# Performance work log

Measured on AMD Instinct MI355X. Metric: run time of the kernel, lower is better.

## Reference

```python
import jax, jax.numpy as jnp
import numpy as np

NUM_HEADS = 16


def setup_inputs() -> dict:
    key = jax.random.key(0)
    ks = jax.random.split(key, 5)
    N, L, E = 4, 1024, 1024
    x = jax.random.normal(ks[0], (N, L, E), dtype=jnp.float32)
    sc = 1.0 / np.sqrt(E)
    wq = jax.random.normal(ks[1], (E, E), dtype=jnp.float32) * sc
    wk = jax.random.normal(ks[2], (E, E), dtype=jnp.float32) * sc
    wv = jax.random.normal(ks[3], (E, E), dtype=jnp.float32) * sc
    wo = jax.random.normal(ks[4], (E, E), dtype=jnp.float32) * sc
    return {"x": x, "wq": wq, "wk": wk, "wv": wv, "wo": wo}


def reference(x, wq, wk, wv, wo):
    N, L, E = x.shape
    H = NUM_HEADS
    d = E // H  # d_k = d_v = d_q
    # Linear layers: y = x @ W^T (torch Linear weight is (out, in))
    q = (x @ wq.T).reshape(N, H, L, d)  # NOTE: raw view, matches torch .view
    k = (x @ wk.T).reshape(N, H, L, d)
    v = (x @ wv.T).reshape(N, H, L, d)
    scores = jnp.einsum("nhld,nhmd->nhlm", q, k) / jnp.sqrt(jnp.float32(d))
    # causal mask (dropout is identity in eval / p=0)
    causal = jnp.tril(jnp.ones((L, L), dtype=bool))
    scores = jnp.where(causal, scores, jnp.float32(-jnp.inf))
    attn = jax.nn.softmax(scores, axis=-1)
    wei = jnp.einsum("nhlm,nhmd->nhld", attn, v).reshape(N, L, H * d)
    return wei @ wo.T
```

## Files before the change

kernel.cpp:

```cpp
#include <hip/hip_runtime.h>
#include <hip/hip_bf16.h>

using bf16 = __hip_bfloat16;
typedef __attribute__((ext_vector_type(8))) short bf16x8;
typedef __attribute__((ext_vector_type(4))) float f32x4;

#define MFMA16(a, b, c) __builtin_amdgcn_mfma_f32_16x16x32_bf16(a, b, c, 0, 0, 0)
#define SWZ(row, byteoff) ((byteoff) ^ (((row) & 7) << 4))

__device__ __forceinline__ unsigned short f2b(float f) {
  union { float f; unsigned int u; } c; c.f = f;
  unsigned int r = c.u + 0x7fffu + ((c.u >> 16) & 1u);
  return (unsigned short)(r >> 16);
}
__device__ __forceinline__ float b2f(short b) {
  union { unsigned int u; float f; } c;
  c.u = ((unsigned int)(unsigned short)b) << 16;
  return c.f;
}
__device__ __forceinline__ bf16x8 scale8(bf16x8 v, float s) {
  bf16x8 r;
#pragma unroll
  for (int j = 0; j < 8; ++j) r[j] = (short)f2b(b2f(v[j]) * s);
  return r;
}
__device__ __forceinline__ unsigned cvtpk(float a, float b) {
  unsigned r;
  asm("v_cvt_pk_bf16_f32 %0, %1, %2" : "=v"(r) : "v"(a), "v"(b));
  return r;
}

__device__ __forceinline__ void gload_lds16(const void* g, void* l) {
  __builtin_amdgcn_global_load_lds(
      (const __attribute__((address_space(1))) void*)g,
      (__attribute__((address_space(3))) void*)l, 16, 0, 0);
}

__device__ __forceinline__ void store_out(float* p, float v) { *p = v; }
__device__ __forceinline__ void store_out(bf16* p, float v) {
  *(unsigned short*)p = f2b(v);
}

__global__ __launch_bounds__(256) void cast_all(
    const float* __restrict__ x, const float* __restrict__ wq,
    const float* __restrict__ wk, const float* __restrict__ wv,
    const float* __restrict__ wo,
    unsigned short* __restrict__ xb, unsigned short* __restrict__ wqb,
    unsigned short* __restrict__ wkb, unsigned short* __restrict__ wvb,
    unsigned short* __restrict__ wob) {
  for (int i = blockIdx.x * 256 + threadIdx.x; i < 2097152; i += 2048 * 256) {
    const float* src;
    unsigned short* dst;
    int off;
    if (i < 1048576) {
      src = x; dst = xb; off = i;
    } else {
      int j = i - 1048576;
      int seg = j >> 18;
      off = j & 262143;
      src = (seg == 0) ? wq : (seg == 1) ? wk : (seg == 2) ? wv : wo;
      dst = (seg == 0) ? wqb : (seg == 1) ? wkb : (seg == 2) ? wvb : wob;
    }
    float4 v = reinterpret_cast<const float4*>(src)[off];
    ushort4 o;
    o.x = f2b(v.x); o.y = f2b(v.y); o.z = f2b(v.z); o.w = f2b(v.w);
    reinterpret_cast<ushort4*>(dst)[off] = o;
  }
}

template <typename TOUT>
__device__ __forceinline__ void gemm_tile(const bf16* __restrict__ A,
                                          const bf16* __restrict__ Bt,
                                          TOUT* __restrict__ C, int N, int K,
                                          int bm, int bn) {
  __shared__ bf16 Asm[128 * 64];
  __shared__ bf16 Bsm[128 * 64];
  const int tid = threadIdx.x;
  const int lane = tid & 63;
  const int w = tid >> 6;
  const int wr = w >> 1, wc = w & 1;
  const int fr = lane & 15;
  const int fg = lane >> 4;
  f32x4 acc[4][4] = {};

  const int strow = w * 8 + (lane >> 3);
  const int stcb = (lane & 7) * 16;

  for (int kt = 0; kt < K; kt += 64) {
#pragma unroll
    for (int r = 0; r < 4; ++r) {
      const int row = r * 32 + strow;
      gload_lds16(
          (const char*)(A + (size_t)(bm + row) * K + kt) + SWZ(row, stcb),
          (char*)Asm + (r * 32 + w * 8) * 128);
      gload_lds16(
          (const char*)(Bt + (size_t)row * K + kt) + SWZ(row, stcb),
          (char*)Bsm + (r * 32 + w * 8) * 128);
    }
    __syncthreads();
    bf16x8 afr[4][2], bfr[4][2];
#pragma unroll
    for (int m = 0; m < 4; ++m) {
      const int row = wr * 64 + m * 16 + fr;
      const char* rp = (const char*)Asm + row * 128;
#pragma unroll
      for (int s = 0; s < 2; ++s)
        afr[m][s] = *(const bf16x8*)(rp + SWZ(row, s * 64 + fg * 16));
    }
#pragma unroll
    for (int n = 0; n < 4; ++n) {
      const int row = wc * 64 + n * 16 + fr;
      const char* rp = (const char*)Bsm + row * 128;
#pragma unroll
      for (int s = 0; s < 2; ++s)
        bfr[n][s] = *(const bf16x8*)(rp + SWZ(row, s * 64 + fg * 16));
    }
    __builtin_amdgcn_s_setprio(1);
#pragma unroll
    for (int m = 0; m < 4; ++m)
#pragma unroll
      for (int n = 0; n < 4; ++n) {
        acc[m][n] = MFMA16(afr[m][0], bfr[n][0], acc[m][n]);
        acc[m][n] = MFMA16(afr[m][1], bfr[n][1], acc[m][n]);
      }
    __builtin_amdgcn_s_setprio(0);
    __syncthreads();
  }
#pragma unroll
  for (int m = 0; m < 4; ++m) {
    const int row0 = bm + wr * 64 + m * 16 + (lane >> 4) * 4;
#pragma unroll
    for (int n = 0; n < 4; ++n) {
      const int col = bn + wc * 64 + n * 16 + fr;
#pragma unroll
      for (int r = 0; r < 4; ++r)
        store_out(&C[(size_t)(row0 + r) * N + col], acc[m][n][r]);
    }
  }
}

__global__ __launch_bounds__(256) void gemm_qkv(
    const bf16* __restrict__ A, const bf16* __restrict__ B3,
    bf16* __restrict__ Cq, bf16* __restrict__ Ck, bf16* __restrict__ Cv) {
  const int id = blockIdx.y * 32 + blockIdx.x;
  const int sw = (id & 7) * 96 + (id >> 3);
  const int bm = (sw & 31) * 128;
  const int bnG = (sw >> 5) * 128;
  bf16* C = (bnG < 1024) ? Cq : (bnG < 2048) ? Ck : Cv;
  gemm_tile<bf16>(A, B3 + (size_t)bnG * 1024, C, 1024, 1024, bm, bnG & 1023);
}

__global__ __launch_bounds__(256) void gemm_out64(const bf16* __restrict__ A,
                                                  const bf16* __restrict__ B,
                                                  float* __restrict__ C) {
  __shared__ bf16 Asm[128 * 64];
  __shared__ bf16 Bsm[64 * 64];
  const int id = blockIdx.y * 32 + blockIdx.x;
  const int sw = (id & 7) * 64 + (id >> 3);
  const int bm = (sw & 31) * 128;
  const int bn = (sw >> 5) * 64;
  const bf16* Bt = B + (size_t)bn * 1024;

  const int tid = threadIdx.x;
  const int lane = tid & 63;
  const int w = tid >> 6;
  const int wr = w >> 1, wc = w & 1;
  const int fr = lane & 15;
  const int fg = lane >> 4;
  f32x4 acc[4][2] = {};

  const int strow = w * 8 + (lane >> 3);
  const int stcb = (lane & 7) * 16;

  for (int kt = 0; kt < 1024; kt += 64) {
#pragma unroll
    for (int r = 0; r < 4; ++r) {
      const int row = r * 32 + strow;
      gload_lds16(
          (const char*)(A + (size_t)(bm + row) * 1024 + kt) + SWZ(row, stcb),
          (char*)Asm + (r * 32 + w * 8) * 128);
    }
#pragma unroll
    for (int r = 0; r < 2; ++r) {
      const int row = r * 32 + strow;
      gload_lds16(
          (const char*)(Bt + (size_t)row * 1024 + kt) + SWZ(row, stcb),
          (char*)Bsm + (r * 32 + w * 8) * 128);
    }
    __syncthreads();
    bf16x8 afr[4][2], bfr[2][2];
#pragma unroll
    for (int m = 0; m < 4; ++m) {
      const int row = wr * 64 + m * 16 + fr;
      const char* rp = (const char*)Asm + row * 128;
#pragma unroll
      for (int s = 0; s < 2; ++s)
        afr[m][s] = *(const bf16x8*)(rp + SWZ(row, s * 64 + fg * 16));
    }
#pragma unroll
    for (int n = 0; n < 2; ++n) {
      const int row = wc * 32 + n * 16 + fr;
      const char* rp = (const char*)Bsm + row * 128;
#pragma unroll
      for (int s = 0; s < 2; ++s)
        bfr[n][s] = *(const bf16x8*)(rp + SWZ(row, s * 64 + fg * 16));
    }
    __builtin_amdgcn_s_setprio(1);
#pragma unroll
    for (int m = 0; m < 4; ++m)
#pragma unroll
      for (int n = 0; n < 2; ++n) {
        acc[m][n] = MFMA16(afr[m][0], bfr[n][0], acc[m][n]);
        acc[m][n] = MFMA16(afr[m][1], bfr[n][1], acc[m][n]);
      }
    __builtin_amdgcn_s_setprio(0);
    __syncthreads();
  }
#pragma unroll
  for (int m = 0; m < 4; ++m) {
    const int row0 = bm + wr * 64 + m * 16 + fg * 4;
#pragma unroll
    for (int n = 0; n < 2; ++n) {
      const int col = bn + wc * 32 + n * 16 + fr;
#pragma unroll
      for (int r = 0; r < 4; ++r)
        C[(size_t)(row0 + r) * 1024 + col] = acc[m][n][r];
    }
  }
}

__global__ __launch_bounds__(256) void attn_fwd(
    const bf16* __restrict__ Q, const bf16* __restrict__ K,
    const bf16* __restrict__ V, bf16* __restrict__ O) {
  const int nh = blockIdx.x;
  const size_t base = (size_t)nh * 65536;
  const bf16* Qp = Q + base;
  const bf16* Kp = K + base;
  const bf16* Vp = V + base;
  bf16* Op = O + base;
  const int pmap[8] = {0, 1, 2, 3, 6, 7, 4, 5};
  const int p = pmap[blockIdx.y];
  const int qiA = p, qiB = 15 - p;
  const int tid = threadIdx.x;
  const int lane = tid & 63;
  const int w = tid >> 6;
  const int fr = lane & 15;
  const int fg = lane >> 4;

  __shared__ __align__(16) bf16 Ksm[2][2][64 * 64];
  __shared__ __align__(16) bf16 Vts[2][2][64 * 64];

  const float QSC = 0.125f * 1.44269504089f;
  const float MS = 12.0f;
  const int rA0 = qiA * 64 + w * 16;
  const int rB0 = qiB * 64 + w * 16;
  bf16x8 qA[2], qB[2];
#pragma unroll
  for (int ks = 0; ks < 2; ++ks) {
    qA[ks] = scale8(
        *(const bf16x8*)&Qp[(size_t)(rA0 + fr) * 64 + ks * 32 + fg * 8], QSC);
    qB[ks] = scale8(
        *(const bf16x8*)&Qp[(size_t)(rB0 + fr) * 64 + ks * 32 + fg * 8], QSC);
  }

  float sA = 0.f, sB = 0.f;
  f32x4 oA[4], oB[4];
#pragma unroll
  for (int d = 0; d < 4; ++d) {
    oA[d] = (f32x4){0.f, 0.f, 0.f, 0.f};
    oB[d] = (f32x4){0.f, 0.f, 0.f, 0.f};
  }

  const int NKV = qiB + 1;
  const int qloc = w * 16 + fr;

  const int bkv = (tid & 15) * 4;
  const int bd = (tid >> 4) * 4;
  const int sbk = ((bkv >> 5) << 6) + (((bkv >> 2) & 3) << 4) +
                  (((bkv >> 4) & 1) << 3);
  union VU { ushort4 v; unsigned short s[4]; };
  VU v4a[4], v4b[4];

  const int krow = w * 16 + (lane >> 3);
  const int kcb = (lane & 7) * 16;

#define STAGE_K(kt, dst)                                                      \
  {                                                                           \
    _Pragma("unroll") for (int i = 0; i < 2; ++i) {                           \
      const int row = krow + i * 8;                                           \
      gload_lds16((const char*)Kp + ((size_t)((kt)*64 + row) * 128 +          \
                                     SWZ(row, kcb)),                          \
                  (char*)(dst) + (w * 16 + i * 8) * 128);                     \
    }                                                                         \
  }
#define LOAD_V(kt, r)                                                         \
  {                                                                           \
    _Pragma("unroll") for (int j = 0; j < 4; ++j) (r)[j].v =                  \
        *(const ushort4*)(Vp + (size_t)((kt)*64 + bkv + j) * 64 + bd);        \
  }
#define WRITE_V(dst, r)                                                       \
  {                                                                           \
    _Pragma("unroll") for (int i = 0; i < 4; ++i) {                           \
      VU o4;                                                                  \
      _Pragma("unroll") for (int j = 0; j < 4; ++j) o4.s[j] = (r)[j].s[i];    \
      const int row = bd + i;                                                 \
      *(ushort4*)((char*)(dst) + row * 128 + SWZ(row, sbk)) = o4.v;           \
    }                                                                         \
  }

  union PU { bf16x8 v; unsigned u[4]; };

  auto load_kf = [&](const char* kb, bf16x8 (&kf)[4][2]) {
#pragma unroll
    for (int c = 0; c < 4; ++c) {
      const int row = c * 16 + fr;
      const char* rp = kb + row * 128;
      kf[c][0] = *(const bf16x8*)(rp + SWZ(row, fg * 16));
      kf[c][1] = *(const bf16x8*)(rp + SWZ(row, 64 + fg * 16));
    }
  };
  auto load_vf = [&](const char* vb, bf16x8 (&vf)[4][2]) {
#pragma unroll
    for (int d = 0; d < 4; ++d) {
      const int row = d * 16 + fr;
      const char* rp = vb + row * 128;
#pragma unroll
      for (int ks = 0; ks < 2; ++ks)
        vf[d][ks] = *(const bf16x8*)(rp + SWZ(row, ks * 64 + fg * 16));
    }
  };
  auto qk_sm = [&](const bf16x8 (&kf)[4][2], const bf16x8 (&qf)[2], float& s,
                   bool diag, PU (&pa)[2]) {
    f32x4 sc[4];
    __builtin_amdgcn_s_setprio(1);
#pragma unroll
    for (int c = 0; c < 4; ++c) {
      f32x4 acc = (f32x4){0.f, 0.f, 0.f, 0.f};
      acc = MFMA16(kf[c][0], qf[0], acc);
      acc = MFMA16(kf[c][1], qf[1], acc);
      sc[c] = acc;
    }
    __builtin_amdgcn_s_setprio(0);
    float pv[4][4];
#pragma unroll
    for (int c = 0; c < 4; ++c)
#pragma unroll
      for (int r = 0; r < 4; ++r) {
        float sv = sc[c][r];
        if (diag) {
          const int kvloc = c * 16 + fg * 4 + r;
          sv = (kvloc <= qloc) ? sv : -INFINITY;
        }
        const float e = __builtin_amdgcn_exp2f(sv - MS);
        pv[c][r] = e;
        s += e;
      }
#pragma unroll
    for (int ks = 0; ks < 2; ++ks) {
      pa[ks].u[0] = cvtpk(pv[ks * 2][0], pv[ks * 2][1]);
      pa[ks].u[1] = cvtpk(pv[ks * 2][2], pv[ks * 2][3]);
      pa[ks].u[2] = cvtpk(pv[ks * 2 + 1][0], pv[ks * 2 + 1][1]);
      pa[ks].u[3] = cvtpk(pv[ks * 2 + 1][2], pv[ks * 2 + 1][3]);
    }
  };
  auto pv_acc = [&](const PU (&pa)[2], const bf16x8 (&vf)[4][2],
                    f32x4 (&o)[4]) {
    __builtin_amdgcn_s_setprio(1);
#pragma unroll
    for (int d = 0; d < 4; ++d) {
      o[d] = MFMA16(pa[0].v, vf[d][0], o[d]);
      o[d] = MFMA16(pa[1].v, vf[d][1], o[d]);
    }
    __builtin_amdgcn_s_setprio(0);
  };

  auto compute_tile = [&](int kt, const char* kb, const char* vb) {
    const bool aAct = (kt <= qiA);
    bf16x8 kf[4][2], vf[4][2];
    load_kf(kb, kf);
    load_vf(vb, vf);
    PU paA[2], paB[2];
    qk_sm(kf, qB, sB, kt == qiB, paB);
    if (aAct) qk_sm(kf, qA, sA, kt == qiA, paA);
    pv_acc(paB, vf, oB);
    if (aAct) pv_acc(paA, vf, oA);
  };

  auto compute_pair = [&](int kt0, const char* kb0, const char* vb0,
                          const char* kb1, const char* vb1) {
    const int kt1 = kt0 + 1;
    const bool a0 = (kt0 <= qiA), a1 = (kt1 <= qiA);
    bf16x8 kf0[4][2], kf1[4][2];
    load_kf(kb0, kf0);
    load_kf(kb1, kf1);
    PU paB0[2], paB1[2], paA0[2], paA1[2];
    qk_sm(kf0, qB, sB, kt0 == qiB, paB0);
    qk_sm(kf1, qB, sB, kt1 == qiB, paB1);
    if (a0) qk_sm(kf0, qA, sA, kt0 == qiA, paA0);
    if (a1) qk_sm(kf1, qA, sA, kt1 == qiA, paA1);
    bf16x8 vf[4][2];
    load_vf(vb0, vf);
    pv_acc(paB0, vf, oB);
    if (a0) pv_acc(paA0, vf, oA);
    load_vf(vb1, vf);
    pv_acc(paB1, vf, oB);
    if (a1) pv_acc(paA1, vf, oA);
  };

  STAGE_K(0, &Ksm[0][0][0]);
  STAGE_K(1, &Ksm[0][1][0]);
  LOAD_V(0, v4a);
  LOAD_V(1, v4b);
  WRITE_V(&Vts[0][0][0], v4a);
  WRITE_V(&Vts[0][1][0], v4b);
  __syncthreads();

  const int I = (NKV + 1) >> 1;
  for (int it = 0; it < I; ++it) {
    const int kt0 = 2 * it;
    const int b = it & 1;
    const bool more0 = (kt0 + 2 < NKV);
    const bool more1 = (kt0 + 3 < NKV);
    if (more0) {
      STAGE_K(kt0 + 2, &Ksm[b ^ 1][0][0]);
      LOAD_V(kt0 + 2, v4a);
    }
    if (more1) {
      STAGE_K(kt0 + 3, &Ksm[b ^ 1][1][0]);
      LOAD_V(kt0 + 3, v4b);
    }

    if (kt0 + 1 < NKV)
      compute_pair(kt0, (const char*)&Ksm[b][0][0], (const char*)&Vts[b][0][0],
                   (const char*)&Ksm[b][1][0], (const char*)&Vts[b][1][0]);
    else
      compute_tile(kt0, (const char*)&Ksm[b][0][0],
                   (const char*)&Vts[b][0][0]);

    if (more0) WRITE_V(&Vts[b ^ 1][0][0], v4a);
    if (more1) WRITE_V(&Vts[b ^ 1][1][0], v4b);
    __syncthreads();
  }

  sA += __shfl_xor(sA, 16); sA += __shfl_xor(sA, 32);
  sB += __shfl_xor(sB, 16); sB += __shfl_xor(sB, 32);
  float sAo[4], sBo[4];
#pragma unroll
  for (int r = 0; r < 4; ++r) {
    sAo[r] = __shfl(sA, fg * 4 + r);
    sBo[r] = __shfl(sB, fg * 4 + r);
  }

#pragma unroll
  for (int d = 0; d < 4; ++d)
#pragma unroll
    for (int r = 0; r < 4; ++r) {
      const float vA = oA[d][r] / sAo[r];
      const float vB = oB[d][r] / sBo[r];
      *(unsigned short*)&Op[(size_t)(rA0 + fg * 4 + r) * 64 + d * 16 + fr] =
          f2b(vA);
      *(unsigned short*)&Op[(size_t)(rB0 + fg * 4 + r) * 64 + d * 16 + fr] =
          f2b(vB);
    }
#undef STAGE_K
#undef LOAD_V
#undef WRITE_V
}

extern "C" void kernel_launch(void* const* d_in, const int* in_sizes, int n_in,
                              void* d_out, int out_size, void* d_ws,
                              size_t ws_size, hipStream_t stream) {
  const float* x = (const float*)d_in[0];
  const float* wq = (const float*)d_in[1];
  const float* wk = (const float*)d_in[2];
  const float* wv = (const float*)d_in[3];
  const float* wo = (const float*)d_in[4];
  float* out = (float*)d_out;
  char* ws = (char*)d_ws;

  bf16* xb = (bf16*)(ws);
  bf16* wqkv = (bf16*)(ws + (8u << 20));
  bf16* wqb = wqkv;
  bf16* wkb = (bf16*)(ws + (10u << 20));
  bf16* wvb = (bf16*)(ws + (12u << 20));
  bf16* wob = (bf16*)(ws + (14u << 20));
  bf16* qbuf = (bf16*)(ws + (16u << 20));
  bf16* kbuf = (bf16*)(ws + (24u << 20));
  bf16* vbuf = (bf16*)(ws + (32u << 20));
  bf16* weib = (bf16*)(ws);

  cast_all<<<2048, 256, 0, stream>>>(x, wq, wk, wv, wo, (unsigned short*)xb,
                                     (unsigned short*)wqb, (unsigned short*)wkb,
                                     (unsigned short*)wvb, (unsigned short*)wob);
  gemm_qkv<<<dim3(32, 24), 256, 0, stream>>>(xb, wqkv, qbuf, kbuf, vbuf);
  attn_fwd<<<dim3(64, 8), 256, 0, stream>>>(qbuf, kbuf, vbuf, weib);
  gemm_out64<<<dim3(32, 16), 256, 0, stream>>>(weib, wob, out);
}
```

Measured before the change: 84.43 us.

## Drop double-buffered K/V staging in attention to halve shared memory

Replaces the double-buffered K/V shared-memory ring with a single pair of buffers. Loads of the next tiles now happen after compute, behind an extra barrier, so global load latency is no longer overlapped with MFMA work. The block-to-query-pair permutation is also removed. The likely intent is to raise occupancy by cutting LDS use, at the cost of exposed load latency and more synchronisation.

Measured after the change: 85.81 us. Within noise of the previous version (+1.6%).

```diff
diff --git a/kernel.cpp b/kernel.cpp
--- a/kernel.cpp
+++ b/kernel.cpp
@@ -238,8 +238,7 @@
   const bf16* Kp = K + base;
   const bf16* Vp = V + base;
   bf16* Op = O + base;
-  const int pmap[8] = {0, 1, 2, 3, 6, 7, 4, 5};
-  const int p = pmap[blockIdx.y];
+  const int p = blockIdx.y;
   const int qiA = p, qiB = 15 - p;
   const int tid = threadIdx.x;
   const int lane = tid & 63;
@@ -247,8 +246,8 @@
   const int fr = lane & 15;
   const int fg = lane >> 4;
 
-  __shared__ __align__(16) bf16 Ksm[2][2][64 * 64];
-  __shared__ __align__(16) bf16 Vts[2][2][64 * 64];
+  __shared__ __align__(16) bf16 Ksm[2][64 * 64];
+  __shared__ __align__(16) bf16 Vts[2][64 * 64];
 
   const float QSC = 0.125f * 1.44269504089f;
   const float MS = 12.0f;
@@ -407,39 +406,36 @@
     if (a1) pv_acc(paA1, vf, oA);
   };
 
-  STAGE_K(0, &Ksm[0][0][0]);
-  STAGE_K(1, &Ksm[0][1][0]);
+  STAGE_K(0, &Ksm[0][0]);
+  STAGE_K(1, &Ksm[1][0]);
   LOAD_V(0, v4a);
   LOAD_V(1, v4b);
-  WRITE_V(&Vts[0][0][0], v4a);
-  WRITE_V(&Vts[0][1][0], v4b);
+  WRITE_V(&Vts[0][0], v4a);
+  WRITE_V(&Vts[1][0], v4b);
   __syncthreads();
 
   const int I = (NKV + 1) >> 1;
   for (int it = 0; it < I; ++it) {
     const int kt0 = 2 * it;
-    const int b = it & 1;
-    const bool more0 = (kt0 + 2 < NKV);
-    const bool more1 = (kt0 + 3 < NKV);
-    if (more0) {
-      STAGE_K(kt0 + 2, &Ksm[b ^ 1][0][0]);
+
+    if (kt0 + 1 < NKV)
+      compute_pair(kt0, (const char*)&Ksm[0][0], (const char*)&Vts[0][0],
+                   (const char*)&Ksm[1][0], (const char*)&Vts[1][0]);
+    else
+      compute_tile(kt0, (const char*)&Ksm[0][0], (const char*)&Vts[0][0]);
+
+    if (kt0 + 2 < NKV) {
+      __syncthreads();
+      STAGE_K(kt0 + 2, &Ksm[0][0]);
       LOAD_V(kt0 + 2, v4a);
-    }
-    if (more1) {
-      STAGE_K(kt0 + 3, &Ksm[b ^ 1][1][0]);
-      LOAD_V(kt0 + 3, v4b);
-    }
-
-    if (kt0 + 1 < NKV)
-      compute_pair(kt0, (const char*)&Ksm[b][0][0], (const char*)&Vts[b][0][0],
-                   (const char*)&Ksm[b][1][0], (const char*)&Vts[b][1][0]);
-    else
-      compute_tile(kt0, (const char*)&Ksm[b][0][0],
-                   (const char*)&Vts[b][0][0]);
-
-    if (more0) WRITE_V(&Vts[b ^ 1][0][0], v4a);
-    if (more1) WRITE_V(&Vts[b ^ 1][1][0], v4b);
-    __syncthreads();
+      WRITE_V(&Vts[0][0], v4a);
+      if (kt0 + 3 < NKV) {
+        STAGE_K(kt0 + 3, &Ksm[1][0]);
+        LOAD_V(kt0 + 3, v4b);
+        WRITE_V(&Vts[1][0], v4b);
+      }
+      __syncthreads();
+    }
   }
 
   sA += __shfl_xor(sA, 16); sA += __shfl_xor(sA, 32);
```
